# Optimization experiments

Hardware: AMD Instinct MI355X
Metric: run time of the kernel (lower is better)

## Reference

```python
import jax, jax.numpy as jnp
import numpy as np

EMBED = 1024
HEAD = 64
SEQ = 2048
BATCH = 8


def setup_inputs() -> dict:
    key = jax.random.key(0)
    kx, kq, kk, kv = jax.random.split(key, 4)
    x = jax.random.normal(kx, (BATCH, SEQ, EMBED), dtype=jnp.float32)
    # torch nn.Linear weight is [out,in]; we store [in,out] so y = x @ W
    Wq = jax.random.normal(kq, (EMBED, HEAD), dtype=jnp.float32) * (EMBED ** -0.5)
    Wk = jax.random.normal(kk, (EMBED, HEAD), dtype=jnp.float32) * (EMBED ** -0.5)
    Wv = jax.random.normal(kv, (EMBED, HEAD), dtype=jnp.float32) * (EMBED ** -0.5)
    return {"x": x, "Wq": Wq, "Wk": Wk, "Wv": Wv}


def reference(x, Wq, Wk, Wv):
    # x: [B,T,C]; single-head causal attention. Scale uses C (embedding dim),
    # matching the original module's C ** (-0.5). Dropout in eval mode (identity).
    B, T, C = x.shape
    q = x @ Wq  # [B,T,H]
    k = x @ Wk  # [B,T,H]
    v = x @ Wv  # [B,T,H]
    scores = jnp.einsum('bqh,bkh->bqk', q, k) * (C ** -0.5)  # [B,T,T]
    causal = jnp.tril(jnp.ones((T, T), dtype=bool))
    scores = jnp.where(causal, scores, -jnp.inf)
    weights = jax.nn.softmax(scores, axis=-1)
    return jnp.einsum('bqk,bkh->bqh', weights, v)  # [B,T,H]
```

## Files before the change

### kernel.cpp

```cpp
#include <hip/hip_runtime.h>
#include <hip/hip_bf16.h>
#include <math.h>

#define BATCH 8
#define SEQ 2048
#define EMBED 1024
#define HEAD 64
#define NROWS (BATCH*SEQ)

typedef short bf16x8 __attribute__((ext_vector_type(8)));
typedef short bf16x4 __attribute__((ext_vector_type(4)));
typedef float f32x4  __attribute__((ext_vector_type(4)));

__device__ inline short f2bf(float f) {
    __hip_bfloat16 h = __float2bfloat16(f);
    return *(short*)&h;
}
__device__ inline float bf2f(short s) {
    __hip_bfloat16 h = *(__hip_bfloat16*)&s;
    return __bfloat162float(h);
}

#define NSLOT 144
__device__ __host__ inline int triOff(int qt) {
    int g = qt >> 2;
    return 2 * g * (g + 1) + (qt & 3) * (g + 1);
}

__global__ __launch_bounds__(256) void prep_w(
    const float* __restrict__ Wq, const float* __restrict__ Wk,
    const float* __restrict__ Wv, short* __restrict__ wt)
{
    int g    = blockIdx.x * 256 + threadIdx.x;
    int lane = g & 63;
    int frag = g >> 6;
    int k32  = frag & 31;
    int ct   = frag >> 5;
    int col  = ct * 16 + (lane & 15);
    int mm   = col >> 6, cc = col & 63;
    const float* W = (mm == 0) ? Wq : ((mm == 1) ? Wk : Wv);
    int kb = k32 * 32 + (lane >> 4) * 8;
    bf16x8 o;
#pragma unroll
    for (int j = 0; j < 8; j++)
        o[j] = f2bf(W[(size_t)(kb + j) * HEAD + cc]);
    *(bf16x8*)&wt[(size_t)g * 8] = o;
}

#define XS_STRIDE 152
__global__ __launch_bounds__(256) void proj_kernel(
    const float* __restrict__ x, const short* __restrict__ wt,
    short* __restrict__ q, short* __restrict__ k, short* __restrict__ v)
{
    __shared__ short xs[16][XS_STRIDE];

    const int tid  = threadIdx.x;
    const int wave = tid >> 6, lane = tid & 63;
    const int m16  = lane & 15, quad = lane >> 4;
    const int r0   = blockIdx.x * 16;

    f32x4 acc[3];
#pragma unroll
    for (int j = 0; j < 3; j++) acc[j] = (f32x4){0.f, 0.f, 0.f, 0.f};

    const int srow = tid >> 4;
    const int skf  = tid & 15;

    const float* xrow = x + (size_t)(r0 + srow) * EMBED;
    float4 xv0 = *(const float4*)&xrow[skf * 4];
    float4 xv1 = *(const float4*)&xrow[64 + skf * 4];

    for (int c = 0; c < 8; c++) {
        __syncthreads();
        {
            bf16x4 b0, b1;
            b0[0] = f2bf(xv0.x); b0[1] = f2bf(xv0.y);
            b0[2] = f2bf(xv0.z); b0[3] = f2bf(xv0.w);
            b1[0] = f2bf(xv1.x); b1[1] = f2bf(xv1.y);
            b1[2] = f2bf(xv1.z); b1[3] = f2bf(xv1.w);
            *(bf16x4*)&xs[srow][skf * 4]      = b0;
            *(bf16x4*)&xs[srow][64 + skf * 4] = b1;
        }
        __syncthreads();
        if (c < 7) {
            xv0 = *(const float4*)&xrow[(c + 1) * 128 + skf * 4];
            xv1 = *(const float4*)&xrow[(c + 1) * 128 + 64 + skf * 4];
        }
#pragma unroll
        for (int s = 0; s < 4; s++) {
            bf16x8 a0 = *(const bf16x8*)&xs[m16][s * 32 + quad * 8];
            int k32 = c * 4 + s;
#pragma unroll
            for (int j = 0; j < 3; j++) {
                int ct = wave * 3 + j;
                bf16x8 bb = *(const bf16x8*)&wt[(size_t)((ct * 32 + k32) * 64 + lane) * 8];
                acc[j] = __builtin_amdgcn_mfma_f32_16x16x32_bf16(a0, bb, acc[j], 0, 0, 0);
            }
        }
    }

#pragma unroll
    for (int j = 0; j < 3; j++) {
        int gcol = wave * 48 + j * 16 + m16;
        int mm = gcol >> 6, cc = gcol & 63;
        short* op = (mm == 0) ? q : ((mm == 1) ? k : v);
#pragma unroll
        for (int reg = 0; reg < 4; reg++) {
            int row = r0 + quad * 4 + reg;
            op[(size_t)row * HEAD + cc] = f2bf(acc[j][reg]);
        }
    }
}

__global__ __launch_bounds__(256) void attn_kernel(
    const short* __restrict__ qg, const short* __restrict__ kg,
    const short* __restrict__ vg,
    short* __restrict__ pO, float* __restrict__ pl)
{
    __shared__ short ksh[64][88];
    __shared__ short vsh[64][88];
    __shared__ short psh[4][16][88];

    const int qt  = blockIdx.x;
    const int seg = blockIdx.y;
    const int b   = blockIdx.z;
    const int c0  = seg * 4;
    const int c1  = min(seg * 4 + 4, qt + 1);
    if (c0 >= c1) return;

    const int tid  = threadIdx.x;
    const int wave = tid >> 6, lane = tid & 63;
    const int m16  = lane & 15, quad = lane >> 4;
    const float scale = 0.03125f;

    const short* qb = qg + (size_t)b * SEQ * HEAD;
    const short* kb = kg + (size_t)b * SEQ * HEAD;
    const short* vb = vg + (size_t)b * SEQ * HEAD;

    bf16x8 a_q[2];
    {
        const int qrow = qt * 64 + wave * 16 + m16;
        a_q[0] = *(const bf16x8*)&qb[(size_t)qrow * HEAD + quad * 8];
        a_q[1] = *(const bf16x8*)&qb[(size_t)qrow * HEAD + 32 + quad * 8];
    }

    f32x4 o_acc[4];
#pragma unroll
    for (int i = 0; i < 4; i++) o_acc[i] = (f32x4){0.f, 0.f, 0.f, 0.f};
    float lsum[4] = {0.f, 0.f, 0.f, 0.f};

    const int krow = tid >> 3;
    const int ks8  = tid & 7;
    const int vp0  = tid >> 3;
    const int vh0  = (tid & 7) * 8;
    const int vpp  = vp0 ^ ((tid & 7) << 2);

    bf16x8 kr0 = *(const bf16x8*)&kb[(size_t)(c0 * 64 + krow) * HEAD + ks8 * 8];
    bf16x8 kr1 = *(const bf16x8*)&kb[(size_t)(c0 * 64 + 32 + krow) * HEAD + ks8 * 8];
    bf16x8 vr0 = *(const bf16x8*)&vb[(size_t)(c0 * 64 + 2 * vp0) * HEAD + vh0];
    bf16x8 vr1 = *(const bf16x8*)&vb[(size_t)(c0 * 64 + 2 * vp0 + 1) * HEAD + vh0];

    for (int c = c0; c < c1; c++) {
        const int t0 = c * 64;
        __syncthreads();
        {
            *(bf16x8*)&ksh[krow][ks8 * 8]      = kr0;
            *(bf16x8*)&ksh[32 + krow][ks8 * 8] = kr1;
#pragma unroll
            for (int j = 0; j < 8; j++) {
                int hh = vh0 + j;
                int val = (vr0[j] & 0xffff) | (((int)vr1[j]) << 16);
                *(int*)&vsh[hh][vpp * 2] = val;
            }
        }
        __syncthreads();
        if (c + 1 < c1) {
            const int tn = (c + 1) * 64;
            kr0 = *(const bf16x8*)&kb[(size_t)(tn + krow) * HEAD + ks8 * 8];
            kr1 = *(const bf16x8*)&kb[(size_t)(tn + 32 + krow) * HEAD + ks8 * 8];
            vr0 = *(const bf16x8*)&vb[(size_t)(tn + 2 * vp0) * HEAD + vh0];
            vr1 = *(const bf16x8*)&vb[(size_t)(tn + 2 * vp0 + 1) * HEAD + vh0];
        }

        f32x4 s_t[4];
#pragma unroll
        for (int nt = 0; nt < 4; nt++) {
            bf16x8 bk0 = *(const bf16x8*)&ksh[nt * 16 + m16][quad * 8];
            bf16x8 bk1 = *(const bf16x8*)&ksh[nt * 16 + m16][32 + quad * 8];
            f32x4 acc = (f32x4){0.f, 0.f, 0.f, 0.f};
            acc = __builtin_amdgcn_mfma_f32_16x16x32_bf16(a_q[0], bk0, acc, 0, 0, 0);
            acc = __builtin_amdgcn_mfma_f32_16x16x32_bf16(a_q[1], bk1, acc, 0, 0, 0);
            s_t[nt] = acc;
        }

        if (c == qt) {
#pragma unroll
            for (int r = 0; r < 4; r++) {
                const int row = qt * 64 + wave * 16 + quad * 4 + r;
#pragma unroll
                for (int nt = 0; nt < 4; nt++) {
                    int t = t0 + nt * 16 + m16;
                    float p = (t <= row) ? __expf(s_t[nt][r] * scale) : 0.f;
                    lsum[r] += p;
                    psh[wave][quad * 4 + r][nt * 16 + m16] = f2bf(p);
                }
            }
        } else {
#pragma unroll
            for (int r = 0; r < 4; r++) {
#pragma unroll
                for (int nt = 0; nt < 4; nt++) {
                    float p = __expf(s_t[nt][r] * scale);
                    lsum[r] += p;
                    psh[wave][quad * 4 + r][nt * 16 + m16] = f2bf(p);
                }
            }
        }

#pragma unroll
        for (int s = 0; s < 2; s++) {
            bf16x8 a_p = *(const bf16x8*)&psh[wave][m16][s * 32 + quad * 8];
#pragma unroll
            for (int ht = 0; ht < 4; ht++) {
                int hh = ht * 16 + m16;
                int pb = (s * 16 + quad * 4) ^ (((hh >> 3) & 7) << 2);
                bf16x8 b_v = *(const bf16x8*)&vsh[hh][pb * 2];
                o_acc[ht] = __builtin_amdgcn_mfma_f32_16x16x32_bf16(a_p, b_v, o_acc[ht], 0, 0, 0);
            }
        }
    }

#pragma unroll
    for (int r = 0; r < 4; r++) {
#pragma unroll
        for (int off = 8; off >= 1; off >>= 1)
            lsum[r] += __shfl_xor(lsum[r], off, 64);
    }
    const size_t slot  = (size_t)b * NSLOT + triOff(qt) + seg;
    const size_t pbase = slot * 64;
#pragma unroll
    for (int ht = 0; ht < 4; ht++) {
#pragma unroll
        for (int r = 0; r < 4; r++) {
            int rowt = wave * 16 + quad * 4 + r;
            pO[(pbase + rowt) * 64 + ht * 16 + m16] = f2bf(o_acc[ht][r]);
        }
    }
    if (m16 == 0) {
#pragma unroll
        for (int r = 0; r < 4; r++) {
            int rowt = wave * 16 + quad * 4 + r;
            pl[pbase + rowt] = lsum[r];
        }
    }
}

__global__ __launch_bounds__(256) void combine_kernel(
    const short* __restrict__ pO, const float* __restrict__ pl,
    float* __restrict__ out)
{
    int g   = blockIdx.x * 256 + threadIdx.x;
    int h4  = (g & 15) * 4;
    int row = (g >> 4) & 2047;
    int b   = g >> 15;
    int qt  = row >> 6, lr = row & 63;
    int ns  = (qt >> 2) + 1;
    size_t base = (size_t)b * NSLOT + triOff(qt);
    float4 O = {0.f, 0.f, 0.f, 0.f};
    float  L = 0.f;
    for (int s = 0; s < ns; s++) {
        bf16x4 ov = *(const bf16x4*)&pO[((base + s) * 64 + lr) * 64 + h4];
        O.x += bf2f(ov[0]); O.y += bf2f(ov[1]);
        O.z += bf2f(ov[2]); O.w += bf2f(ov[3]);
        L += pl[(base + s) * 64 + lr];
    }
    float inv = 1.f / L;
    O.x *= inv; O.y *= inv; O.z *= inv; O.w *= inv;
    *(float4*)&out[(size_t)g * 4] = O;
}

extern "C" void kernel_launch(void* const* d_in, const int* in_sizes, int n_in,
                              void* d_out, int out_size, void* d_ws, size_t ws_size,
                              hipStream_t stream) {
    const float* x  = (const float*)d_in[0];
    const float* Wq = (const float*)d_in[1];
    const float* Wk = (const float*)d_in[2];
    const float* Wv = (const float*)d_in[3];
    float* out = (float*)d_out;

    short* q  = (short*)d_ws;
    short* k  = q + (size_t)NROWS * HEAD;
    short* v  = k + (size_t)NROWS * HEAD;
    short* wt = v + (size_t)NROWS * HEAD;
    short* pO = wt + 196608;
    float* pl = (float*)(pO + (size_t)BATCH * NSLOT * 64 * 64);

    prep_w<<<96, 256, 0, stream>>>(Wq, Wk, Wv, wt);
    proj_kernel<<<1024, 256, 0, stream>>>(x, wt, q, k, v);
    attn_kernel<<<dim3(32, 8, 8), 256, 0, stream>>>(q, k, v, pO, pl);
    combine_kernel<<<1024, 256, 0, stream>>>(pO, pl, out);
}
```

Measured before the change: 138.2 us.

## Restructure projection kernel: 32-row tiles, full-K LDS staging, split-K waves

The projection kernel now handles 32 rows per block with 512 threads. It loads the whole 1024-wide x slice into LDS up front, converted to bf16 with an XOR swizzle to avoid bank conflicts. Each weight fragment is reused across two 16-row M tiles, and the K dimension is split between two wave groups whose partial sums are reduced through LDS. The goal is to halve weight-fragment global loads per row and remove the per-chunk double-barrier loop. The cost is 64KB of LDS per block, which limits occupancy, and the load phase is no longer overlapped with compute.

```diff
diff --git a/kernel.cpp b/kernel.cpp
--- a/kernel.cpp
+++ b/kernel.cpp
@@ -47,68 +47,91 @@
     *(bf16x8*)&wt[(size_t)g * 8] = o;
 }
 
-#define XS_STRIDE 152
-__global__ __launch_bounds__(256) void proj_kernel(
+__global__ __launch_bounds__(512, 4) void proj_kernel(
     const float* __restrict__ x, const short* __restrict__ wt,
     short* __restrict__ q, short* __restrict__ k, short* __restrict__ v)
 {
-    __shared__ short xs[16][XS_STRIDE];
+    __shared__ short xs[32][1024];
+    float* psum = (float*)&xs[0][0];
 
     const int tid  = threadIdx.x;
     const int wave = tid >> 6, lane = tid & 63;
     const int m16  = lane & 15, quad = lane >> 4;
-    const int r0   = blockIdx.x * 16;
-
-    f32x4 acc[3];
-#pragma unroll
-    for (int j = 0; j < 3; j++) acc[j] = (f32x4){0.f, 0.f, 0.f, 0.f};
-
-    const int srow = tid >> 4;
-    const int skf  = tid & 15;
-
-    const float* xrow = x + (size_t)(r0 + srow) * EMBED;
-    float4 xv0 = *(const float4*)&xrow[skf * 4];
-    float4 xv1 = *(const float4*)&xrow[64 + skf * 4];
-
-    for (int c = 0; c < 8; c++) {
-        __syncthreads();
-        {
-            bf16x4 b0, b1;
-            b0[0] = f2bf(xv0.x); b0[1] = f2bf(xv0.y);
-            b0[2] = f2bf(xv0.z); b0[3] = f2bf(xv0.w);
-            b1[0] = f2bf(xv1.x); b1[1] = f2bf(xv1.y);
-            b1[2] = f2bf(xv1.z); b1[3] = f2bf(xv1.w);
-            *(bf16x4*)&xs[srow][skf * 4]      = b0;
-            *(bf16x4*)&xs[srow][64 + skf * 4] = b1;
-        }
-        __syncthreads();
-        if (c < 7) {
-            xv0 = *(const float4*)&xrow[(c + 1) * 128 + skf * 4];
-            xv1 = *(const float4*)&xrow[(c + 1) * 128 + 64 + skf * 4];
-        }
-#pragma unroll
-        for (int s = 0; s < 4; s++) {
-            bf16x8 a0 = *(const bf16x8*)&xs[m16][s * 32 + quad * 8];
-            int k32 = c * 4 + s;
+    const int cg   = wave & 3;
+    const int kh   = wave >> 2;
+    const int r0   = blockIdx.x * 32;
+
+    {
+        const int row  = tid >> 4;
+        const int col4 = tid & 15;
+        const float* xr = x + (size_t)(r0 + row) * EMBED;
+#pragma unroll
+        for (int h = 0; h < 2; h++) {
+            float4 f[8];
+#pragma unroll
+            for (int i = 0; i < 8; i++)
+                f[i] = *(const float4*)&xr[(h * 8 + i) * 64 + col4 * 4];
+#pragma unroll
+            for (int i = 0; i < 8; i++) {
+                int c  = (h * 8 + i) * 64 + col4 * 4;
+                int k8 = c >> 3, rem = c & 7;
+                int cs = ((k8 ^ (row & 7)) << 3) + rem;
+                bf16x4 bv;
+                bv[0] = f2bf(f[i].x); bv[1] = f2bf(f[i].y);
+                bv[2] = f2bf(f[i].z); bv[3] = f2bf(f[i].w);
+                *(bf16x4*)&xs[row][cs] = bv;
+            }
+        }
+    }
+    __syncthreads();
+
+    f32x4 acc[2][3];
+#pragma unroll
+    for (int mt = 0; mt < 2; mt++)
+#pragma unroll
+        for (int j = 0; j < 3; j++) acc[mt][j] = (f32x4){0.f, 0.f, 0.f, 0.f};
+
+#pragma unroll 4
+    for (int s = 0; s < 16; s++) {
+        int k32  = kh * 16 + s;
+        int ksw  = ((k32 * 4 + quad) ^ (m16 & 7)) << 3;
+        bf16x8 a0 = *(const bf16x8*)&xs[m16][ksw];
+        bf16x8 a1 = *(const bf16x8*)&xs[16 + m16][ksw];
+#pragma unroll
+        for (int j = 0; j < 3; j++) {
+            int ct = cg * 3 + j;
+            bf16x8 bb = *(const bf16x8*)&wt[(size_t)((ct * 32 + k32) * 64 + lane) * 8];
+            acc[0][j] = __builtin_amdgcn_mfma_f32_16x16x32_bf16(a0, bb, acc[0][j], 0, 0, 0);
+            acc[1][j] = __builtin_amdgcn_mfma_f32_16x16x32_bf16(a1, bb, acc[1][j], 0, 0, 0);
+        }
+    }
+
+    __syncthreads();
+    if (kh == 1) {
+        float* p = psum + ((size_t)(cg * 64 + lane) * 24);
+#pragma unroll
+        for (int mt = 0; mt < 2; mt++)
+#pragma unroll
+            for (int j = 0; j < 3; j++)
+                *(f32x4*)&p[(mt * 3 + j) * 4] = acc[mt][j];
+    }
+    __syncthreads();
+    if (kh == 0) {
+        const float* p = psum + ((size_t)(cg * 64 + lane) * 24);
+#pragma unroll
+        for (int mt = 0; mt < 2; mt++)
 #pragma unroll
             for (int j = 0; j < 3; j++) {
-                int ct = wave * 3 + j;
-                bf16x8 bb = *(const bf16x8*)&wt[(size_t)((ct * 32 + k32) * 64 + lane) * 8];
-                acc[j] = __builtin_amdgcn_mfma_f32_16x16x32_bf16(a0, bb, acc[j], 0, 0, 0);
-            }
-        }
-    }
-
-#pragma unroll
-    for (int j = 0; j < 3; j++) {
-        int gcol = wave * 48 + j * 16 + m16;
-        int mm = gcol >> 6, cc = gcol & 63;
-        short* op = (mm == 0) ? q : ((mm == 1) ? k : v);
-#pragma unroll
-        for (int reg = 0; reg < 4; reg++) {
-            int row = r0 + quad * 4 + reg;
-            op[(size_t)row * HEAD + cc] = f2bf(acc[j][reg]);
-        }
+                f32x4 o = acc[mt][j] + *(const f32x4*)&p[(mt * 3 + j) * 4];
+                int gcol = (cg * 3 + j) * 16 + m16;
+                int mm = gcol >> 6, cc = gcol & 63;
+                short* op = (mm == 0) ? q : ((mm == 1) ? k : v);
+#pragma unroll
+                for (int reg = 0; reg < 4; reg++) {
+                    int row = r0 + mt * 16 + quad * 4 + reg;
+                    op[(size_t)row * HEAD + cc] = f2bf(o[reg]);
+                }
+            }
     }
 }
 
@@ -296,7 +319,7 @@
     float* pl = (float*)(pO + (size_t)BATCH * NSLOT * 64 * 64);
 
     prep_w<<<96, 256, 0, stream>>>(Wq, Wk, Wv, wt);
-    proj_kernel<<<1024, 256, 0, stream>>>(x, wt, q, k, v);
+    proj_kernel<<<512, 512, 0, stream>>>(x, wt, q, k, v);
     attn_kernel<<<dim3(32, 8, 8), 256, 0, stream>>>(q, k, v, pO, pl);
     combine_kernel<<<1024, 256, 0, stream>>>(pO, pl, out);
 }
```

New measurement: 128.9 us. 6.8% less time.
